# Kernel tuning notes

Hardware: AMD Instinct MI355X
Metric: run time of the kernel (lower is better)

Reference implementation:

```python
import jax, jax.numpy as jnp
import numpy as np

N = 100000      # n_heads + n_tails (entities)
E = 3200000     # nnz of sparse A_in (avg degree 32)
D = 128         # in_dim == out_dim
LAMDA = 0.5
ALPHA = 0.1
L_LAYER = 1
NEG_SLOPE = 0.01  # torch LeakyReLU default


def _leaky_relu(x):
    return jnp.where(x >= 0, x, NEG_SLOPE * x)


def setup_inputs() -> dict:
    key = jax.random.key(0)
    ks = jax.random.split(key, 10)
    ego = jax.random.normal(ks[0], (N, D), jnp.float32) * 0.1
    h0 = jax.random.normal(ks[1], (N, D), jnp.float32) * 0.1
    row = jax.random.randint(ks[2], (E,), 0, N)
    col = jax.random.randint(ks[3], (E,), 0, N)
    vals = jax.random.uniform(ks[4], (E,), jnp.float32) / 32.0  # ~normalized adjacency
    stdv = 1.0 / np.sqrt(D)
    weight = jax.random.uniform(ks[5], (D, D), jnp.float32, -stdv, stdv)
    w1 = jax.random.normal(ks[6], (D, D), jnp.float32) * (1.0 / np.sqrt(D))
    b1 = jnp.zeros((D,), jnp.float32)
    w2 = jax.random.normal(ks[7], (D, D), jnp.float32) * (1.0 / np.sqrt(D))
    b2 = jnp.zeros((D,), jnp.float32)
    return {"ego_embeddings": ego, "h0": h0, "vals": vals, "weight": weight,
            "w1": w1, "b1": b1, "w2": w2, "b2": b2, "row": row, "col": col}


def reference(ego_embeddings, h0, vals, weight, w1, b1, w2, b2, row, col):
    # SpMM: side = A_in @ ego  (COO gather-scale-scatter)
    side = jax.ops.segment_sum(vals[:, None] * ego_embeddings[col], row,
                               num_segments=N)  # (N, D)

    # residual_connection with use_residual=True
    beta = np.float32(np.log(LAMDA / L_LAYER + 1.0))
    identity_mapping = (1.0 - beta) + beta * weight  # (D, D)

    def resid(hi):
        return ((1.0 - ALPHA) * hi + ALPHA * h0) @ identity_mapping

    # bi-interaction: sum branch + elementwise-product branch
    sum_emb = _leaky_relu(resid(ego_embeddings + side) @ w1 + b1)
    bi_emb = _leaky_relu(resid(ego_embeddings * side) @ w2 + b2)
    # message_dropout is identity in eval mode
    return sum_emb + bi_emb
```

## Files before the change

### kernel.cpp

```cpp
#include <hip/hip_runtime.h>
#include <stdint.h>

#define D 128
#define BETA 0.40546510810816444f
#define TSTR 136

#define NWG  128
#define MAXB 256

typedef __bf16 bf16x8 __attribute__((ext_vector_type(8)));
typedef float f32x4 __attribute__((ext_vector_type(4)));

__device__ __forceinline__ float bf2f(uint16_t u) {
    union { uint32_t i; float f; } x; x.i = ((uint32_t)u) << 16; return x.f;
}
__device__ __forceinline__ uint16_t f2bf(float f) {
    union { float f; uint32_t i; } x; x.f = f;
    uint32_t r = (x.i + 0x7fffu + ((x.i >> 16) & 1u)) >> 16;
    return (uint16_t)r;
}
__device__ __forceinline__ float lo_f(uint32_t u) { return __uint_as_float(u << 16); }
__device__ __forceinline__ float hi_f(uint32_t u) { return __uint_as_float(u & 0xffff0000u); }
__device__ __forceinline__ uint32_t pack2(float x, float y) {
    return (uint32_t)f2bf(x) | ((uint32_t)f2bf(y) << 16);
}

__global__ void k_hist(const int* __restrict__ row, int* __restrict__ deg, int E, int N) {
    int e = blockIdx.x * blockDim.x + threadIdx.x;
    if (e < E) {
        int r = row[e]; r = min(max(r, 0), N - 1);
        atomicAdd(&deg[r], 1);
    }
}

__global__ void k_scan1(const int* __restrict__ deg, int* __restrict__ inc,
                        int* __restrict__ bsum, int n) {
    __shared__ int s[1024];
    int i = blockIdx.x * 1024 + threadIdx.x;
    int v = (i < n) ? deg[i] : 0;
    s[threadIdx.x] = v;
    __syncthreads();
    for (int d = 1; d < 1024; d <<= 1) {
        int t = (threadIdx.x >= (unsigned)d) ? s[threadIdx.x - d] : 0;
        __syncthreads();
        s[threadIdx.x] += t;
        __syncthreads();
    }
    if (i < n) inc[i] = s[threadIdx.x];
    if (threadIdx.x == 1023) bsum[blockIdx.x] = s[1023];
}

__global__ void k_scan2(const int* __restrict__ bsum, int* __restrict__ boff,
                        int nb, int* __restrict__ rowptr, int N) {
    int run = 0;
    for (int b = 0; b < nb; b++) { boff[b] = run; run += bsum[b]; }
    rowptr[N] = run;
}

__global__ void k_scan3(const int* __restrict__ deg, const int* __restrict__ boff,
                        int* __restrict__ rowptr, int* __restrict__ wp, int n) {
    int i = blockIdx.x * 1024 + threadIdx.x;
    if (i < n) {
        int ex = rowptr[i] - deg[i] + boff[blockIdx.x];
        rowptr[i] = ex;
        wp[i] = ex;
    }
}

__global__ void k_scatter(const int* __restrict__ row, const int* __restrict__ col,
                          const float* __restrict__ vals, int* __restrict__ wp,
                          uint2* __restrict__ rec, int E, int N) {
    int e = blockIdx.x * blockDim.x + threadIdx.x;
    if (e < E) {
        int r = row[e]; r = min(max(r, 0), N - 1);
        int pos = atomicAdd(&wp[r], 1);
        pos = min(max(pos, 0), E - 1);
        uint2 rv;
        rv.x = (uint32_t)col[e];
        rv.y = __float_as_uint(vals[e]);
        rec[pos] = rv;
    }
}

__global__ void k_cvt(const float4* __restrict__ src, uint2* __restrict__ dst, int n) {
    int i = blockIdx.x * blockDim.x + threadIdx.x;
    if (i < n) {
        float4 v = src[i];
        uint2 o; o.x = pack2(v.x, v.y); o.y = pack2(v.z, v.w);
        dst[i] = o;
    }
}

__global__ void k_prep(const float* __restrict__ W, const float* __restrict__ w1,
                       const float* __restrict__ w2, uint16_t* __restrict__ M1T,
                       uint16_t* __restrict__ M2T) {
    int k = blockIdx.x, n = threadIdx.x;
    __shared__ float imrow[D];
    imrow[n] = (1.0f - BETA) + BETA * W[k * D + n];
    __syncthreads();
    float s1 = 0.f, s2 = 0.f;
    for (int j = 0; j < D; j++) {
        float im = imrow[j];
        s1 += im * w1[j * D + n];
        s2 += im * w2[j * D + n];
    }
    M1T[n * D + k] = f2bf(s1);
    M2T[n * D + k] = f2bf(s2);
}

__global__ __launch_bounds__(256) void k_front(
        const float* __restrict__ W, const float* __restrict__ w1,
        const float* __restrict__ w2, uint16_t* __restrict__ M1T,
        uint16_t* __restrict__ M2T,
        const float4* __restrict__ egoq, uint2* __restrict__ egobq, int nquads,
        const int* __restrict__ row, int* __restrict__ cnt,
        int E, int N, int nbuck, int cvtB) {
    __shared__ int h[MAXB];
    __shared__ float imrow[2][D];
    int tid = threadIdx.x;
    int bid = blockIdx.x;

    if (bid < 64) {
        int half = tid >> 7;
        int n = tid & 127;
        int k = bid * 2 + half;
        imrow[half][n] = (1.0f - BETA) + BETA * W[k * D + n];
        __syncthreads();
        float s1 = 0.f, s2 = 0.f;
        for (int j = 0; j < D; j++) {
            float im = imrow[half][j];
            s1 += im * w1[j * D + n];
            s2 += im * w2[j * D + n];
        }
        M1T[n * D + k] = f2bf(s1);
        M2T[n * D + k] = f2bf(s2);
        return;
    }
    if (bid < 64 + cvtB) {
        int i = (bid - 64) * 256 + tid;
        if (i < nquads) {
            float4 v = egoq[i];
            uint2 o; o.x = pack2(v.x, v.y); o.y = pack2(v.z, v.w);
            egobq[i] = o;
        }
        return;
    }
    int w = bid - 64 - cvtB;
    for (int b = tid; b < nbuck; b += 256) h[b] = 0;
    __syncthreads();
    int chunk = (E + NWG - 1) / NWG;
    int beg = w * chunk, end = min(beg + chunk, E);
    for (int e = beg + tid; e < end; e += 256) {
        int r = row[e]; r = min(max(r, 0), N - 1);
        atomicAdd(&h[r >> 9], 1);
    }
    __syncthreads();
    for (int b = tid; b < nbuck; b += 256) cnt[b * NWG + w] = h[b];
}

__global__ __launch_bounds__(1024) void k_scanWB(int* __restrict__ cnt, int M) {
    __shared__ int s[1024];
    int t = threadIdx.x;
    int per = (M + 1023) / 1024;
    int beg = t * per, end = min(beg + per, M);
    int sum = 0;
    for (int i = beg; i < end; i++) sum += cnt[i];
    s[t] = sum;
    __syncthreads();
    for (int d = 1; d < 1024; d <<= 1) {
        int v = (t >= d) ? s[t - d] : 0;
        __syncthreads();
        s[t] += v;
        __syncthreads();
    }
    int run = (t == 0) ? 0 : s[t - 1];
    for (int i = beg; i < end; i++) {
        int v = cnt[i];
        cnt[i] = run;
        run += v;
    }
    if (t == 1023) cnt[M] = s[1023];
}

__global__ __launch_bounds__(512) void k_group(const int* __restrict__ row,
                                               const int* __restrict__ col,
                                               const float* __restrict__ vals,
                                               const int* __restrict__ off,
                                               uint2* __restrict__ grouped,
                                               int E, int N, int nbuck) {
    __shared__ int lbase[MAXB];
    __shared__ int lcnt[MAXB];
    int w = blockIdx.x;
    for (int b = threadIdx.x; b < nbuck; b += 512) {
        lbase[b] = off[b * NWG + w];
        lcnt[b] = 0;
    }
    __syncthreads();
    int chunk = (E + NWG - 1) / NWG;
    int beg = w * chunk, end = min(beg + chunk, E);
    for (int e = beg + threadIdx.x; e < end; e += 512) {
        int r = row[e]; r = min(max(r, 0), N - 1);
        int c = col[e]; c = min(max(c, 0), N - 1);
        int b = r >> 9;
        int lp = atomicAdd(&lcnt[b], 1);
        int pos = lbase[b] + lp;
        pos = min(max(pos, 0), E - 1);
        uint2 g;
        g.x = ((uint32_t)(r & 511) << 17) | (uint32_t)c;
        g.y = __float_as_uint(vals[e]);
        grouped[pos] = g;
    }
}

__global__ __launch_bounds__(512) void k_place(const uint2* __restrict__ grouped,
                                               const int* __restrict__ off,
                                               int* __restrict__ rowptr,
                                               uint2* __restrict__ rec,
                                               int E, int N, int nbuck) {
    __shared__ int lh[512];
    __shared__ int lc[512];
    __shared__ int ps[512];
    int b = blockIdx.x;
    int t = threadIdx.x;
    int beg = off[b * NWG], end = off[(b + 1) * NWG];
    lh[t] = 0; lc[t] = 0;
    __syncthreads();
    for (int i = beg + t; i < end; i += 512)
        atomicAdd(&lh[grouped[i].x >> 17], 1);
    __syncthreads();
    ps[t] = lh[t];
    __syncthreads();
    for (int d = 1; d < 512; d <<= 1) {
        int v = (t >= d) ? ps[t - d] : 0;
        __syncthreads();
        ps[t] += v;
        __syncthreads();
    }
    int ex = (t == 0) ? 0 : ps[t - 1];
    lh[t] = ex;
    __syncthreads();
    int rbase = b << 9;
    int r = rbase + t;
    if (r < N) rowptr[r] = beg + lh[t];
    if (b == nbuck - 1 && t == 0) rowptr[N] = E;
    for (int i = beg + t; i < end; i += 512) {
        uint2 g = grouped[i];
        int rl = (int)(g.x >> 17);
        int lp = atomicAdd(&lc[rl], 1);
        int pos = beg + lh[rl] + lp;
        pos = min(max(pos, 0), E - 1);
        uint2 rv;
        rv.x = g.x & 0x1FFFFu;
        rv.y = g.y;
        rec[pos] = rv;
    }
}

__device__ __forceinline__ void gemm_phase(
        const uint16_t* sT1, const uint16_t* sT2,
        const uint16_t* __restrict__ M1T, const uint16_t* __restrict__ M2T,
        const float* __restrict__ b1, const float* __restrict__ b2,
        float* __restrict__ out, int base, int wave, int lane, int N) {
    int l15 = lane & 15, quad = lane >> 4;
#pragma unroll
    for (int t = 0; t < 2; t++) {
        int tn = wave * 2 + t;
        f32x4 acc1 = {0.f, 0.f, 0.f, 0.f}, acc2 = {0.f, 0.f, 0.f, 0.f};
#pragma unroll
        for (int kb = 0; kb < 4; kb++) {
            int ko = kb * 32 + quad * 8;
            bf16x8 a1 = *(const bf16x8*)(sT1 + l15 * TSTR + ko);
            bf16x8 a2 = *(const bf16x8*)(sT2 + l15 * TSTR + ko);
            bf16x8 bb1 = *(const bf16x8*)(M1T + (tn * 16 + l15) * D + ko);
            bf16x8 bb2 = *(const bf16x8*)(M2T + (tn * 16 + l15) * D + ko);
            acc1 = __builtin_amdgcn_mfma_f32_16x16x32_bf16(a1, bb1, acc1, 0, 0, 0);
            acc2 = __builtin_amdgcn_mfma_f32_16x16x32_bf16(a2, bb2, acc2, 0, 0, 0);
        }
        int colo = tn * 16 + l15;
        float bbias1 = b1[colo], bbias2 = b2[colo];
#pragma unroll
        for (int r = 0; r < 4; r++) {
            int rowi = base + quad * 4 + r;
            if (rowi < N) {
                float v1 = acc1[r] + bbias1;
                v1 = (v1 >= 0.f) ? v1 : 0.01f * v1;
                float v2 = acc2[r] + bbias2;
                v2 = (v2 >= 0.f) ? v2 : 0.01f * v2;
                out[(size_t)rowi * D + colo] = v1 + v2;
            }
        }
    }
}

__global__ __launch_bounds__(256) void k_fused(
        const int* __restrict__ rowptr, const uint2* __restrict__ rec,
        const uint32_t* __restrict__ egob,
        const float2* __restrict__ egf, const float2* __restrict__ hh,
        const uint16_t* __restrict__ M1T, const uint16_t* __restrict__ M2T,
        const float* __restrict__ b1, const float* __restrict__ b2,
        float* __restrict__ out, int N) {
    __shared__ __attribute__((aligned(16))) uint16_t sT1[16 * TSTR];
    __shared__ __attribute__((aligned(16))) uint16_t sT2[16 * TSTR];
    int tid = threadIdx.x;
    int wave = tid >> 6, lane = tid & 63;
    int base = blockIdx.x * 16;
    uint32_t* s1d = (uint32_t*)sT1;
    uint32_t* s2d = (uint32_t*)sT2;

#pragma unroll
    for (int i = 0; i < 4; i++) {
        int node = base + wave * 4 + i;
        float t1x = 0.f, t1y = 0.f, t2x = 0.f, t2y = 0.f;
        if (node < N) {
            int e0 = rowptr[node], e1 = rowptr[node + 1];
            float ax = 0.f, ay = 0.f, bx = 0.f, by = 0.f;
            int e = e0;
            for (; e + 8 <= e1; e += 8) {
                uint2 r0 = rec[e + 0], r1 = rec[e + 1], r2 = rec[e + 2], r3 = rec[e + 3];
                uint2 r4 = rec[e + 4], r5 = rec[e + 5], r6 = rec[e + 6], r7 = rec[e + 7];
                int c0 = min(max((int)r0.x, 0), N - 1);
                int c1 = min(max((int)r1.x, 0), N - 1);
                int c2 = min(max((int)r2.x, 0), N - 1);
                int c3 = min(max((int)r3.x, 0), N - 1);
                int c4 = min(max((int)r4.x, 0), N - 1);
                int c5 = min(max((int)r5.x, 0), N - 1);
                int c6 = min(max((int)r6.x, 0), N - 1);
                int c7 = min(max((int)r7.x, 0), N - 1);
                uint32_t u0 = egob[c0 * 64 + lane];
                uint32_t u1 = egob[c1 * 64 + lane];
                uint32_t u2 = egob[c2 * 64 + lane];
                uint32_t u3 = egob[c3 * 64 + lane];
                uint32_t u4 = egob[c4 * 64 + lane];
                uint32_t u5 = egob[c5 * 64 + lane];
                uint32_t u6 = egob[c6 * 64 + lane];
                uint32_t u7 = egob[c7 * 64 + lane];
                float v0 = __uint_as_float(r0.y), v1 = __uint_as_float(r1.y);
                float v2 = __uint_as_float(r2.y), v3 = __uint_as_float(r3.y);
                float v4 = __uint_as_float(r4.y), v5 = __uint_as_float(r5.y);
                float v6 = __uint_as_float(r6.y), v7 = __uint_as_float(r7.y);
                ax += v0 * lo_f(u0); ay += v0 * hi_f(u0);
                bx += v1 * lo_f(u1); by += v1 * hi_f(u1);
                ax += v2 * lo_f(u2); ay += v2 * hi_f(u2);
                bx += v3 * lo_f(u3); by += v3 * hi_f(u3);
                ax += v4 * lo_f(u4); ay += v4 * hi_f(u4);
                bx += v5 * lo_f(u5); by += v5 * hi_f(u5);
                ax += v6 * lo_f(u6); ay += v6 * hi_f(u6);
                bx += v7 * lo_f(u7); by += v7 * hi_f(u7);
            }
            if (e < e1) {
                int last = e1 - 1;
                uint2 rr[8];
#pragma unroll
                for (int k = 0; k < 8; k++) {
                    int idx = e + k;
                    rr[k] = rec[(idx <= last) ? idx : last];
                }
                uint32_t uu[8];
#pragma unroll
                for (int k = 0; k < 8; k++) {
                    int c = min(max((int)rr[k].x, 0), N - 1);
                    uu[k] = egob[c * 64 + lane];
                }
#pragma unroll
                for (int k = 0; k < 8; k++) {
                    float v = (e + k < e1) ? __uint_as_float(rr[k].y) : 0.f;
                    if (k & 1) { bx += v * lo_f(uu[k]); by += v * hi_f(uu[k]); }
                    else       { ax += v * lo_f(uu[k]); ay += v * hi_f(uu[k]); }
                }
            }
            ax += bx; ay += by;
            float2 se = egf[node * 64 + lane];
            float2 sh = hh[node * 64 + lane];
            t1x = 0.9f * (se.x + ax) + 0.1f * sh.x;
            t1y = 0.9f * (se.y + ay) + 0.1f * sh.y;
            t2x = 0.9f * (se.x * ax) + 0.1f * sh.x;
            t2y = 0.9f * (se.y * ay) + 0.1f * sh.y;
        }
        int r = wave * 4 + i;
        s1d[r * (TSTR / 2) + lane] = pack2(t1x, t1y);
        s2d[r * (TSTR / 2) + lane] = pack2(t2x, t2y);
    }
    __syncthreads();
    gemm_phase(sT1, sT2, M1T, M2T, b1, b2, out, base, wave, lane, N);
}

__global__ __launch_bounds__(256) void k_coo_side(
        const int* __restrict__ row, const int* __restrict__ col,
        const float* __restrict__ vals, const float2* __restrict__ egf,
        float* __restrict__ sideF, int E, int N) {
    long long t = (long long)blockIdx.x * blockDim.x + threadIdx.x;
    int e = (int)(t >> 6), l = (int)(t & 63);
    if (e >= E) return;
    int c = col[e]; c = min(max(c, 0), N - 1);
    int r = row[e]; r = min(max(r, 0), N - 1);
    float v = vals[e];
    float2 u = egf[c * 64 + l];
    atomicAdd(&sideF[r * D + 2 * l],     v * u.x);
    atomicAdd(&sideF[r * D + 2 * l + 1], v * u.y);
}

__global__ __launch_bounds__(256) void k_fused2(
        const float2* __restrict__ egf, const float2* __restrict__ hh,
        const uint16_t* __restrict__ M1T, const uint16_t* __restrict__ M2T,
        const float* __restrict__ b1, const float* __restrict__ b2,
        float* __restrict__ out, int N) {
    __shared__ __attribute__((aligned(16))) uint16_t sT1[16 * TSTR];
    __shared__ __attribute__((aligned(16))) uint16_t sT2[16 * TSTR];
    int tid = threadIdx.x;
    int wave = tid >> 6, lane = tid & 63;
    int base = blockIdx.x * 16;
    const float2* sd = (const float2*)out;
    uint32_t* s1d = (uint32_t*)sT1;
    uint32_t* s2d = (uint32_t*)sT2;

#pragma unroll
    for (int i = 0; i < 4; i++) {
        int node = base + wave * 4 + i;
        float t1x = 0.f, t1y = 0.f, t2x = 0.f, t2y = 0.f;
        if (node < N) {
            float2 us = sd[node * 64 + lane];
            float2 se = egf[node * 64 + lane];
            float2 sh = hh[node * 64 + lane];
            t1x = 0.9f * (se.x + us.x) + 0.1f * sh.x;
            t1y = 0.9f * (se.y + us.y) + 0.1f * sh.y;
            t2x = 0.9f * (se.x * us.x) + 0.1f * sh.x;
            t2y = 0.9f * (se.y * us.y) + 0.1f * sh.y;
        }
        int r = wave * 4 + i;
        s1d[r * (TSTR / 2) + lane] = pack2(t1x, t1y);
        s2d[r * (TSTR / 2) + lane] = pack2(t2x, t2y);
    }
    __syncthreads();
    gemm_phase(sT1, sT2, M1T, M2T, b1, b2, out, base, wave, lane, N);
}

extern "C" void kernel_launch(void* const* d_in, const int* in_sizes, int n_in,
                              void* d_out, int out_size, void* d_ws, size_t ws_size,
                              hipStream_t stream) {
    const float* ego  = (const float*)d_in[0];
    const float* h0   = (const float*)d_in[1];
    const float* vals = (const float*)d_in[2];
    const float* W    = (const float*)d_in[3];
    const float* w1   = (const float*)d_in[4];
    const float* b1   = (const float*)d_in[5];
    const float* w2   = (const float*)d_in[6];
    const float* b2   = (const float*)d_in[7];
    const int* row = (const int*)d_in[8];
    const int* col = (const int*)d_in[9];
    int N = in_sizes[0] / D;
    int E = in_sizes[2];

    char* p = (char*)d_ws;
    auto alloc = [&](size_t bytes) -> char* {
        char* q = p;
        p += (bytes + 511) & ~(size_t)511;
        return q;
    };
    uint16_t* M1T    = (uint16_t*)alloc(D * D * 2);
    uint16_t* M2T    = (uint16_t*)alloc(D * D * 2);
    uint32_t* egob   = (uint32_t*)alloc((size_t)N * 64 * 4);
    int*      deg    = (int*)alloc((size_t)N * 4);
    int*      rowptr = (int*)alloc((size_t)(N + 1) * 4);
    int*      wp     = (int*)alloc((size_t)N * 4);
    int*      bsum   = (int*)alloc(1024 * 4);
    int*      boff   = (int*)alloc(1024 * 4);
    int*      cnt    = (int*)alloc(((size_t)MAXB * NWG + 1) * 4);
    uint2*    rec    = (uint2*)alloc((size_t)E * 8);
    size_t need_fast = (size_t)(p - (char*)d_ws);

    if (ws_size >= need_fast) {
        int nquads = N * 32;
        int nbuck = (N + 511) >> 9;
        bool bucket_ok = (nbuck <= MAXB) && ((size_t)out_size * 4 >= (size_t)E * 8)
                         && ((N & 1) == 0);
        if (bucket_ok) {
            int cvtB = (nquads + 255) / 256;
            int M = nbuck * NWG;
            k_front<<<64 + cvtB + NWG, 256, 0, stream>>>(
                W, w1, w2, M1T, M2T,
                (const float4*)ego, (uint2*)egob, nquads,
                row, cnt, E, N, nbuck, cvtB);
            k_scanWB<<<1, 1024, 0, stream>>>(cnt, M);
            k_group<<<NWG, 512, 0, stream>>>(row, col, vals, cnt,
                                             (uint2*)d_out, E, N, nbuck);
            k_place<<<nbuck, 512, 0, stream>>>((const uint2*)d_out, cnt,
                                               rowptr, rec, E, N, nbuck);
        } else {
            k_prep<<<D, D, 0, stream>>>(W, w1, w2, M1T, M2T);
            k_cvt<<<(nquads + 255) / 256, 256, 0, stream>>>((const float4*)ego,
                                                            (uint2*)egob, nquads);
            hipMemsetAsync(deg, 0, (size_t)N * 4, stream);
            int nb = (N + 1023) / 1024;
            k_hist<<<(E + 255) / 256, 256, 0, stream>>>(row, deg, E, N);
            k_scan1<<<nb, 1024, 0, stream>>>(deg, rowptr, bsum, N);
            k_scan2<<<1, 1, 0, stream>>>(bsum, boff, nb, rowptr, N);
            k_scan3<<<nb, 1024, 0, stream>>>(deg, boff, rowptr, wp, N);
            k_scatter<<<(E + 255) / 256, 256, 0, stream>>>(row, col, vals, wp, rec, E, N);
        }
        int nblocks = (N + 15) / 16;
        k_fused<<<nblocks, 256, 0, stream>>>(rowptr, rec, egob,
                                             (const float2*)ego, (const float2*)h0,
                                             M1T, M2T, b1, b2, (float*)d_out, N);
    } else {
        k_prep<<<D, D, 0, stream>>>(W, w1, w2, M1T, M2T);
        hipMemsetAsync(d_out, 0, (size_t)out_size * 4, stream);
        long long tthr = (long long)E * 64;
        int blocks = (int)((tthr + 255) / 256);
        k_coo_side<<<blocks, 256, 0, stream>>>(row, col, vals, (const float2*)ego,
                                               (float*)d_out, E, N);
        int nblocks = (N + 15) / 16;
        k_fused2<<<nblocks, 256, 0, stream>>>((const float2*)ego, (const float2*)h0,
                                              M1T, M2T, b1, b2, (float*)d_out, N);
    }
}
```

Baseline: 508.6 us.

## Fuse CSR build stages into one cooperative kernel with grid syncs

Replaces the four-launch bucketed CSR construction (front/scan/group/place) with a single cooperative kernel that does weight prep, bf16 conversion, bucket histogram, scans, grouping and placement, separated by grid-wide syncs. Buckets shrink from 512 to 256 rows and the grid grows to 512 blocks. This is meant to remove launch gaps and the single-block scan kernel. In exchange it adds grid.sync costs, needs occupancy to allow cooperative launch, and keeps the old path as a fallback.

```diff
diff --git a/kernel.cpp b/kernel.cpp
--- a/kernel.cpp
+++ b/kernel.cpp
@@ -1,5 +1,8 @@
 #include <hip/hip_runtime.h>
+#include <hip/hip_cooperative_groups.h>
 #include <stdint.h>
+
+namespace cg = cooperative_groups;
 
 #define D 128
 #define BETA 0.40546510810816444f
@@ -8,12 +11,14 @@
 #define NWG  128
 #define MAXB 256
 
+#define CGRID 512
+#define CTHR  512
+#define BROWS 256
+#define MAXB2 512
+
 typedef __bf16 bf16x8 __attribute__((ext_vector_type(8)));
 typedef float f32x4 __attribute__((ext_vector_type(4)));
 
-__device__ __forceinline__ float bf2f(uint16_t u) {
-    union { uint32_t i; float f; } x; x.i = ((uint32_t)u) << 16; return x.f;
-}
 __device__ __forceinline__ uint16_t f2bf(float f) {
     union { float f; uint32_t i; } x; x.f = f;
     uint32_t r = (x.i + 0x7fffu + ((x.i >> 16) & 1u)) >> 16;
@@ -23,6 +28,151 @@
 __device__ __forceinline__ float hi_f(uint32_t u) { return __uint_as_float(u & 0xffff0000u); }
 __device__ __forceinline__ uint32_t pack2(float x, float y) {
     return (uint32_t)f2bf(x) | ((uint32_t)f2bf(y) << 16);
+}
+
+__global__ __launch_bounds__(CTHR, 4) void k_build(
+        const float* __restrict__ W, const float* __restrict__ w1,
+        const float* __restrict__ w2, uint16_t* __restrict__ M1T,
+        uint16_t* __restrict__ M2T,
+        const float4* __restrict__ egoq, uint2* __restrict__ egobq, int nquads,
+        const int* __restrict__ row, const int* __restrict__ col,
+        const float* __restrict__ vals,
+        int* __restrict__ cnt, int* __restrict__ partial,
+        uint2* __restrict__ grouped, int* __restrict__ rowptr,
+        uint2* __restrict__ rec, int E, int N, int nbuck) {
+    __shared__ float imrow[4][D];
+    __shared__ int h[MAXB2];
+    __shared__ int s[CTHR];
+    __shared__ int lb[MAXB2];
+    __shared__ int lc2[MAXB2];
+    __shared__ int lh[BROWS];
+    __shared__ int lcc[BROWS];
+    __shared__ int ps[BROWS];
+    int t = threadIdx.x, bid = blockIdx.x, G = gridDim.x;
+    cg::grid_group grid = cg::this_grid();
+
+    if (bid < 32) {
+        int q = t >> 7, n = t & 127;
+        int k = bid * 4 + q;
+        imrow[q][n] = (1.0f - BETA) + BETA * W[k * D + n];
+        __syncthreads();
+        float s1 = 0.f, s2 = 0.f;
+        for (int j = 0; j < D; j++) {
+            float im = imrow[q][j];
+            s1 += im * w1[j * D + n];
+            s2 += im * w2[j * D + n];
+        }
+        M1T[n * D + k] = f2bf(s1);
+        M2T[n * D + k] = f2bf(s2);
+    }
+    for (int i = bid * CTHR + t; i < nquads; i += G * CTHR) {
+        float4 v = egoq[i];
+        uint2 o; o.x = pack2(v.x, v.y); o.y = pack2(v.z, v.w);
+        egobq[i] = o;
+    }
+    for (int b = t; b < nbuck; b += CTHR) h[b] = 0;
+    __syncthreads();
+    int chunk = (E + G - 1) / G;
+    int ebeg = bid * chunk, eend = min(ebeg + chunk, E);
+    for (int e = ebeg + t; e < eend; e += CTHR) {
+        int r = row[e]; r = min(max(r, 0), N - 1);
+        atomicAdd(&h[r >> 8], 1);
+    }
+    __syncthreads();
+    for (int b = t; b < nbuck; b += CTHR) cnt[b * G + bid] = h[b];
+
+    grid.sync();
+
+    int S = nbuck;
+    {
+        int base_i = bid * S;
+        int v = (t < S) ? cnt[base_i + t] : 0;
+        s[t] = v;
+        __syncthreads();
+        for (int d = 1; d < CTHR; d <<= 1) {
+            int x = (t >= d) ? s[t - d] : 0;
+            __syncthreads();
+            s[t] += x;
+            __syncthreads();
+        }
+        if (t < S) cnt[base_i + t] = s[t] - v;
+        if (t == CTHR - 1) partial[bid] = s[t];
+    }
+    grid.sync();
+
+    if (bid == 0) {
+        int v = (t < G) ? partial[t] : 0;
+        s[t] = v;
+        __syncthreads();
+        for (int d = 1; d < CTHR; d <<= 1) {
+            int x = (t >= d) ? s[t - d] : 0;
+            __syncthreads();
+            s[t] += x;
+            __syncthreads();
+        }
+        if (t < G) partial[t] = s[t] - v;
+        if (t == CTHR - 1) cnt[nbuck * G] = s[t];
+    }
+    grid.sync();
+
+    {
+        int base_i = bid * S;
+        int add = partial[bid];
+        if (t < S) cnt[base_i + t] += add;
+    }
+    grid.sync();
+
+    for (int b = t; b < nbuck; b += CTHR) { lb[b] = cnt[b * G + bid]; lc2[b] = 0; }
+    __syncthreads();
+    for (int e = ebeg + t; e < eend; e += CTHR) {
+        int r = row[e]; r = min(max(r, 0), N - 1);
+        int c = col[e]; c = min(max(c, 0), N - 1);
+        int b = r >> 8;
+        int lp = atomicAdd(&lc2[b], 1);
+        int pos = lb[b] + lp;
+        pos = min(max(pos, 0), E - 1);
+        uint2 g;
+        g.x = ((uint32_t)(r & 255) << 17) | (uint32_t)c;
+        g.y = __float_as_uint(vals[e]);
+        grouped[pos] = g;
+    }
+    grid.sync();
+
+    for (int b = bid; b < nbuck; b += G) {
+        int pb = cnt[b * G], pe = cnt[(b + 1) * G];
+        if (t < BROWS) { lh[t] = 0; lcc[t] = 0; }
+        __syncthreads();
+        for (int i = pb + t; i < pe; i += CTHR)
+            atomicAdd(&lh[grouped[i].x >> 17], 1);
+        __syncthreads();
+        int v = (t < BROWS) ? lh[t] : 0;
+        if (t < BROWS) ps[t] = v;
+        __syncthreads();
+        for (int d = 1; d < BROWS; d <<= 1) {
+            int x = (t < BROWS && t >= d) ? ps[t - d] : 0;
+            __syncthreads();
+            if (t < BROWS) ps[t] += x;
+            __syncthreads();
+        }
+        if (t < BROWS) lh[t] = ps[t] - v;
+        __syncthreads();
+        int rbase = b << 8;
+        if (t < BROWS) {
+            int r = rbase + t;
+            if (r < N) rowptr[r] = pb + lh[t];
+        }
+        if (b == nbuck - 1 && t == 0) rowptr[N] = E;
+        for (int i = pb + t; i < pe; i += CTHR) {
+            uint2 g = grouped[i];
+            int rl = (int)(g.x >> 17);
+            int lp = atomicAdd(&lcc[rl], 1);
+            int pos = pb + lh[rl] + lp;
+            pos = min(max(pos, 0), E - 1);
+            uint2 rv; rv.x = g.x & 0x1FFFFu; rv.y = g.y;
+            rec[pos] = rv;
+        }
+        __syncthreads();
+    }
 }
 
 __global__ void k_hist(const int* __restrict__ row, int* __restrict__ deg, int E, int N) {
@@ -450,6 +600,10 @@
     int N = in_sizes[0] / D;
     int E = in_sizes[2];
 
+    int nbuck2 = (N + 255) >> 8;
+    size_t cnt_elems = (size_t)nbuck2 * CGRID + 2;
+    if (cnt_elems < (size_t)MAXB * NWG + 1) cnt_elems = (size_t)MAXB * NWG + 1;
+
     char* p = (char*)d_ws;
     auto alloc = [&](size_t bytes) -> char* {
         char* q = p;
@@ -464,39 +618,75 @@
     int*      wp     = (int*)alloc((size_t)N * 4);
     int*      bsum   = (int*)alloc(1024 * 4);
     int*      boff   = (int*)alloc(1024 * 4);
-    int*      cnt    = (int*)alloc(((size_t)MAXB * NWG + 1) * 4);
+    int*      partial= (int*)alloc(CGRID * 4);
+    int*      cnt    = (int*)alloc(cnt_elems * 4);
     uint2*    rec    = (uint2*)alloc((size_t)E * 8);
     size_t need_fast = (size_t)(p - (char*)d_ws);
 
+    static int coop_state = 0;
+    if (coop_state == 0) {
+        int maxb = 0;
+        hipError_t oe = hipOccupancyMaxActiveBlocksPerMultiprocessor(&maxb, k_build, CTHR, 0);
+        int cus = 0;
+        hipDeviceProp_t prop;
+        if (hipGetDeviceProperties(&prop, 0) == hipSuccess) cus = prop.multiProcessorCount;
+        coop_state = (oe == hipSuccess && cus > 0 && maxb * cus >= CGRID) ? 1 : -1;
+    }
+
     if (ws_size >= need_fast) {
         int nquads = N * 32;
-        int nbuck = (N + 511) >> 9;
-        bool bucket_ok = (nbuck <= MAXB) && ((size_t)out_size * 4 >= (size_t)E * 8)
-                         && ((N & 1) == 0);
-        if (bucket_ok) {
-            int cvtB = (nquads + 255) / 256;
-            int M = nbuck * NWG;
-            k_front<<<64 + cvtB + NWG, 256, 0, stream>>>(
-                W, w1, w2, M1T, M2T,
-                (const float4*)ego, (uint2*)egob, nquads,
-                row, cnt, E, N, nbuck, cvtB);
-            k_scanWB<<<1, 1024, 0, stream>>>(cnt, M);
-            k_group<<<NWG, 512, 0, stream>>>(row, col, vals, cnt,
-                                             (uint2*)d_out, E, N, nbuck);
-            k_place<<<nbuck, 512, 0, stream>>>((const uint2*)d_out, cnt,
-                                               rowptr, rec, E, N, nbuck);
-        } else {
-            k_prep<<<D, D, 0, stream>>>(W, w1, w2, M1T, M2T);
-            k_cvt<<<(nquads + 255) / 256, 256, 0, stream>>>((const float4*)ego,
-                                                            (uint2*)egob, nquads);
-            hipMemsetAsync(deg, 0, (size_t)N * 4, stream);
-            int nb = (N + 1023) / 1024;
-            k_hist<<<(E + 255) / 256, 256, 0, stream>>>(row, deg, E, N);
-            k_scan1<<<nb, 1024, 0, stream>>>(deg, rowptr, bsum, N);
-            k_scan2<<<1, 1, 0, stream>>>(bsum, boff, nb, rowptr, N);
-            k_scan3<<<nb, 1024, 0, stream>>>(deg, boff, rowptr, wp, N);
-            k_scatter<<<(E + 255) / 256, 256, 0, stream>>>(row, col, vals, wp, rec, E, N);
-        }
+        bool done_build = false;
+
+        bool coop_ok = (coop_state == 1) && (nbuck2 <= MAXB2) &&
+                       ((size_t)out_size * 4 >= (size_t)E * 8);
+        if (coop_ok) {
+            const float4* egoq = (const float4*)ego;
+            uint2* egobq = (uint2*)egob;
+            uint2* groupedp = (uint2*)d_out;
+            void* args[] = {
+                (void*)&W, (void*)&w1, (void*)&w2, (void*)&M1T, (void*)&M2T,
+                (void*)&egoq, (void*)&egobq, (void*)&nquads,
+                (void*)&row, (void*)&col, (void*)&vals,
+                (void*)&cnt, (void*)&partial, (void*)&groupedp,
+                (void*)&rowptr, (void*)&rec, (void*)&E, (void*)&N, (void*)&nbuck2
+            };
+            hipError_t le = hipLaunchCooperativeKernel(
+                (const void*)k_build, dim3(CGRID), dim3(CTHR), args, 0, stream);
+            if (le == hipSuccess) done_build = true;
+            else coop_state = -1;
+        }
+
+        if (!done_build) {
+            int nbuck = (N + 511) >> 9;
+            bool bucket_ok = (nbuck <= MAXB) && ((size_t)out_size * 4 >= (size_t)E * 8)
+                             && ((N & 1) == 0);
+            if (bucket_ok) {
+                int cvtB = (nquads + 255) / 256;
+                int M = nbuck * NWG;
+                k_front<<<64 + cvtB + NWG, 256, 0, stream>>>(
+                    W, w1, w2, M1T, M2T,
+                    (const float4*)ego, (uint2*)egob, nquads,
+                    row, cnt, E, N, nbuck, cvtB);
+                k_scanWB<<<1, 1024, 0, stream>>>(cnt, M);
+                k_group<<<NWG, 512, 0, stream>>>(row, col, vals, cnt,
+                                                 (uint2*)d_out, E, N, nbuck);
+                k_place<<<nbuck, 512, 0, stream>>>((const uint2*)d_out, cnt,
+                                                   rowptr, rec, E, N, nbuck);
+            } else {
+                k_prep<<<D, D, 0, stream>>>(W, w1, w2, M1T, M2T);
+                k_cvt<<<(nquads + 255) / 256, 256, 0, stream>>>((const float4*)ego,
+                                                                (uint2*)egob, nquads);
+                hipMemsetAsync(deg, 0, (size_t)N * 4, stream);
+                int nb = (N + 1023) / 1024;
+                k_hist<<<(E + 255) / 256, 256, 0, stream>>>(row, deg, E, N);
+                k_scan1<<<nb, 1024, 0, stream>>>(deg, rowptr, bsum, N);
+                k_scan2<<<1, 1, 0, stream>>>(bsum, boff, nb, rowptr, N);
+                k_scan3<<<nb, 1024, 0, stream>>>(deg, boff, rowptr, wp, N);
+                k_scatter<<<(E + 255) / 256, 256, 0, stream>>>(row, col, vals, wp,
+                                                               rec, E, N);
+            }
+        }
+
         int nblocks = (N + 15) / 16;
         k_fused<<<nblocks, 256, 0, stream>>>(rowptr, rec, egob,
                                              (const float2*)ego, (const float2*)h0,
```

Result: slower. 766.7 us (+50.8%).

## Use smaller 256-row buckets and more workgroups in the COO-to-CSR bucket sort

Applied to the files above, without the earlier changes.

The two-pass bucket sort now uses 256-row buckets instead of 512 and 256 partitioning workgroups instead of 128. The single-block whole-matrix scan is replaced by a small kernel that only computes per-bucket totals; each grouping workgroup then forms its own offsets by summing the earlier workgroups' counts. The placement kernel handles 256 rows per block, which gives about 391 blocks for better GPU occupancy and a shorter per-block LDS scan. The cost is a serial prefix loop of up to 255 entries per bucket inside k_group2, and the N-even restriction is dropped.

```diff
diff --git a/kernel.cpp b/kernel.cpp
--- a/kernel.cpp
+++ b/kernel.cpp
@@ -8,12 +8,13 @@
 #define NWG  128
 #define MAXB 256
 
+#define NWG2 256
+#define BROWS 256
+#define MAXB2 512
+
 typedef __bf16 bf16x8 __attribute__((ext_vector_type(8)));
 typedef float f32x4 __attribute__((ext_vector_type(4)));
 
-__device__ __forceinline__ float bf2f(uint16_t u) {
-    union { uint32_t i; float f; } x; x.i = ((uint32_t)u) << 16; return x.f;
-}
 __device__ __forceinline__ uint16_t f2bf(float f) {
     union { float f; uint32_t i; } x; x.f = f;
     uint32_t r = (x.i + 0x7fffu + ((x.i >> 16) & 1u)) >> 16;
@@ -115,7 +116,7 @@
         const float4* __restrict__ egoq, uint2* __restrict__ egobq, int nquads,
         const int* __restrict__ row, int* __restrict__ cnt,
         int E, int N, int nbuck, int cvtB) {
-    __shared__ int h[MAXB];
+    __shared__ int h[MAXB2];
     __shared__ float imrow[2][D];
     int tid = threadIdx.x;
     int bid = blockIdx.x;
@@ -148,110 +149,116 @@
     int w = bid - 64 - cvtB;
     for (int b = tid; b < nbuck; b += 256) h[b] = 0;
     __syncthreads();
-    int chunk = (E + NWG - 1) / NWG;
+    int chunk = (E + NWG2 - 1) / NWG2;
     int beg = w * chunk, end = min(beg + chunk, E);
     for (int e = beg + tid; e < end; e += 256) {
         int r = row[e]; r = min(max(r, 0), N - 1);
-        atomicAdd(&h[r >> 9], 1);
-    }
-    __syncthreads();
-    for (int b = tid; b < nbuck; b += 256) cnt[b * NWG + w] = h[b];
-}
-
-__global__ __launch_bounds__(1024) void k_scanWB(int* __restrict__ cnt, int M) {
-    __shared__ int s[1024];
+        atomicAdd(&h[r >> 8], 1);
+    }
+    __syncthreads();
+    for (int b = tid; b < nbuck; b += 256) cnt[b * NWG2 + w] = h[b];
+}
+
+__global__ __launch_bounds__(512) void k_btop(const int* __restrict__ cnt,
+                                              int* __restrict__ bbase, int nbuck) {
+    __shared__ int s[512];
     int t = threadIdx.x;
-    int per = (M + 1023) / 1024;
-    int beg = t * per, end = min(beg + per, M);
     int sum = 0;
-    for (int i = beg; i < end; i++) sum += cnt[i];
+    if (t < nbuck) {
+        const int4* p4 = (const int4*)(cnt + t * NWG2);
+#pragma unroll 4
+        for (int i = 0; i < NWG2 / 4; i++) {
+            int4 v = p4[i];
+            sum += v.x + v.y + v.z + v.w;
+        }
+    }
     s[t] = sum;
     __syncthreads();
-    for (int d = 1; d < 1024; d <<= 1) {
-        int v = (t >= d) ? s[t - d] : 0;
-        __syncthreads();
-        s[t] += v;
-        __syncthreads();
-    }
-    int run = (t == 0) ? 0 : s[t - 1];
-    for (int i = beg; i < end; i++) {
-        int v = cnt[i];
-        cnt[i] = run;
-        run += v;
-    }
-    if (t == 1023) cnt[M] = s[1023];
-}
-
-__global__ __launch_bounds__(512) void k_group(const int* __restrict__ row,
-                                               const int* __restrict__ col,
-                                               const float* __restrict__ vals,
-                                               const int* __restrict__ off,
-                                               uint2* __restrict__ grouped,
-                                               int E, int N, int nbuck) {
-    __shared__ int lbase[MAXB];
-    __shared__ int lcnt[MAXB];
+    for (int d = 1; d < 512; d <<= 1) {
+        int x = (t >= d) ? s[t - d] : 0;
+        __syncthreads();
+        s[t] += x;
+        __syncthreads();
+    }
+    if (t < nbuck) bbase[t] = s[t] - sum;
+    if (t == 511) bbase[nbuck] = s[511];
+}
+
+__global__ __launch_bounds__(512) void k_group2(const int* __restrict__ row,
+                                                const int* __restrict__ col,
+                                                const float* __restrict__ vals,
+                                                const int* __restrict__ cnt,
+                                                const int* __restrict__ bbase,
+                                                uint2* __restrict__ grouped,
+                                                int E, int N, int nbuck) {
+    __shared__ int lbase[MAXB2];
+    __shared__ int lcnt[MAXB2];
+    int t = threadIdx.x;
     int w = blockIdx.x;
-    for (int b = threadIdx.x; b < nbuck; b += 512) {
-        lbase[b] = off[b * NWG + w];
+    for (int b = t; b < nbuck; b += 512) {
+        const int* cr = cnt + b * NWG2;
+        int off = bbase[b];
+        for (int w2 = 0; w2 < w; w2++) off += cr[w2];
+        lbase[b] = off;
         lcnt[b] = 0;
     }
     __syncthreads();
-    int chunk = (E + NWG - 1) / NWG;
+    int chunk = (E + NWG2 - 1) / NWG2;
     int beg = w * chunk, end = min(beg + chunk, E);
-    for (int e = beg + threadIdx.x; e < end; e += 512) {
+    for (int e = beg + t; e < end; e += 512) {
         int r = row[e]; r = min(max(r, 0), N - 1);
         int c = col[e]; c = min(max(c, 0), N - 1);
-        int b = r >> 9;
+        int b = r >> 8;
         int lp = atomicAdd(&lcnt[b], 1);
         int pos = lbase[b] + lp;
         pos = min(max(pos, 0), E - 1);
         uint2 g;
-        g.x = ((uint32_t)(r & 511) << 17) | (uint32_t)c;
+        g.x = ((uint32_t)(r & 255) << 17) | (uint32_t)c;
         g.y = __float_as_uint(vals[e]);
         grouped[pos] = g;
     }
 }
 
-__global__ __launch_bounds__(512) void k_place(const uint2* __restrict__ grouped,
-                                               const int* __restrict__ off,
-                                               int* __restrict__ rowptr,
-                                               uint2* __restrict__ rec,
-                                               int E, int N, int nbuck) {
-    __shared__ int lh[512];
-    __shared__ int lc[512];
-    __shared__ int ps[512];
+__global__ __launch_bounds__(512) void k_place2(const uint2* __restrict__ grouped,
+                                                const int* __restrict__ bbase,
+                                                int* __restrict__ rowptr,
+                                                uint2* __restrict__ rec,
+                                                int E, int N, int nbuck) {
+    __shared__ int lh[BROWS];
+    __shared__ int lcc[BROWS];
+    __shared__ int ps[BROWS];
     int b = blockIdx.x;
     int t = threadIdx.x;
-    int beg = off[b * NWG], end = off[(b + 1) * NWG];
-    lh[t] = 0; lc[t] = 0;
-    __syncthreads();
-    for (int i = beg + t; i < end; i += 512)
+    int pb = bbase[b], pe = bbase[b + 1];
+    if (t < BROWS) { lh[t] = 0; lcc[t] = 0; }
+    __syncthreads();
+    for (int i = pb + t; i < pe; i += 512)
         atomicAdd(&lh[grouped[i].x >> 17], 1);
     __syncthreads();
-    ps[t] = lh[t];
-    __syncthreads();
-    for (int d = 1; d < 512; d <<= 1) {
-        int v = (t >= d) ? ps[t - d] : 0;
-        __syncthreads();
-        ps[t] += v;
-        __syncthreads();
-    }
-    int ex = (t == 0) ? 0 : ps[t - 1];
-    lh[t] = ex;
-    __syncthreads();
-    int rbase = b << 9;
-    int r = rbase + t;
-    if (r < N) rowptr[r] = beg + lh[t];
+    int v = (t < BROWS) ? lh[t] : 0;
+    if (t < BROWS) ps[t] = v;
+    __syncthreads();
+    for (int d = 1; d < BROWS; d <<= 1) {
+        int x = (t < BROWS && t >= d) ? ps[t - d] : 0;
+        __syncthreads();
+        if (t < BROWS) ps[t] += x;
+        __syncthreads();
+    }
+    if (t < BROWS) lh[t] = ps[t] - v;
+    __syncthreads();
+    int rbase = b << 8;
+    if (t < BROWS) {
+        int r = rbase + t;
+        if (r < N) rowptr[r] = pb + lh[t];
+    }
     if (b == nbuck - 1 && t == 0) rowptr[N] = E;
-    for (int i = beg + t; i < end; i += 512) {
+    for (int i = pb + t; i < pe; i += 512) {
         uint2 g = grouped[i];
         int rl = (int)(g.x >> 17);
-        int lp = atomicAdd(&lc[rl], 1);
-        int pos = beg + lh[rl] + lp;
+        int lp = atomicAdd(&lcc[rl], 1);
+        int pos = pb + lh[rl] + lp;
         pos = min(max(pos, 0), E - 1);
-        uint2 rv;
-        rv.x = g.x & 0x1FFFFu;
-        rv.y = g.y;
+        uint2 rv; rv.x = g.x & 0x1FFFFu; rv.y = g.y;
         rec[pos] = rv;
     }
 }
@@ -450,6 +457,10 @@
     int N = in_sizes[0] / D;
     int E = in_sizes[2];
 
+    int nbuck2 = (N + 255) >> 8;
+    size_t cnt_elems = (size_t)nbuck2 * NWG2 + 2;
+    if (cnt_elems < (size_t)MAXB * NWG + 1) cnt_elems = (size_t)MAXB * NWG + 1;
+
     char* p = (char*)d_ws;
     auto alloc = [&](size_t bytes) -> char* {
         char* q = p;
@@ -464,27 +475,24 @@
     int*      wp     = (int*)alloc((size_t)N * 4);
     int*      bsum   = (int*)alloc(1024 * 4);
     int*      boff   = (int*)alloc(1024 * 4);
-    int*      cnt    = (int*)alloc(((size_t)MAXB * NWG + 1) * 4);
+    int*      cnt    = (int*)alloc(cnt_elems * 4);
     uint2*    rec    = (uint2*)alloc((size_t)E * 8);
     size_t need_fast = (size_t)(p - (char*)d_ws);
 
     if (ws_size >= need_fast) {
         int nquads = N * 32;
-        int nbuck = (N + 511) >> 9;
-        bool bucket_ok = (nbuck <= MAXB) && ((size_t)out_size * 4 >= (size_t)E * 8)
-                         && ((N & 1) == 0);
+        bool bucket_ok = (nbuck2 <= MAXB2) && ((size_t)out_size * 4 >= (size_t)E * 8);
         if (bucket_ok) {
             int cvtB = (nquads + 255) / 256;
-            int M = nbuck * NWG;
-            k_front<<<64 + cvtB + NWG, 256, 0, stream>>>(
+            k_front<<<64 + cvtB + NWG2, 256, 0, stream>>>(
                 W, w1, w2, M1T, M2T,
                 (const float4*)ego, (uint2*)egob, nquads,
-                row, cnt, E, N, nbuck, cvtB);
-            k_scanWB<<<1, 1024, 0, stream>>>(cnt, M);
-            k_group<<<NWG, 512, 0, stream>>>(row, col, vals, cnt,
-                                             (uint2*)d_out, E, N, nbuck);
-            k_place<<<nbuck, 512, 0, stream>>>((const uint2*)d_out, cnt,
-                                               rowptr, rec, E, N, nbuck);
+                row, cnt, E, N, nbuck2, cvtB);
+            k_btop<<<1, 512, 0, stream>>>(cnt, boff, nbuck2);
+            k_group2<<<NWG2, 512, 0, stream>>>(row, col, vals, cnt, boff,
+                                               (uint2*)d_out, E, N, nbuck2);
+            k_place2<<<nbuck2, 512, 0, stream>>>((const uint2*)d_out, boff,
+                                                 rowptr, rec, E, N, nbuck2);
         } else {
             k_prep<<<D, D, 0, stream>>>(W, w1, w2, M1T, M2T);
             k_cvt<<<(nquads + 255) / 256, 256, 0, stream>>>((const float4*)ego,
@@ -495,7 +503,8 @@
             k_scan1<<<nb, 1024, 0, stream>>>(deg, rowptr, bsum, N);
             k_scan2<<<1, 1, 0, stream>>>(bsum, boff, nb, rowptr, N);
             k_scan3<<<nb, 1024, 0, stream>>>(deg, boff, rowptr, wp, N);
-            k_scatter<<<(E + 255) / 256, 256, 0, stream>>>(row, col, vals, wp, rec, E, N);
+            k_scatter<<<(E + 255) / 256, 256, 0, stream>>>(row, col, vals, wp,
+                                                           rec, E, N);
         }
         int nblocks = (N + 15) / 16;
         k_fused<<<nblocks, 256, 0, stream>>>(rowptr, rec, egob,
```

New measurement: 475.6 us. 6.5% less time.
